# Optimization experiments

Hardware: AMD Instinct MI355X
Metric: run time of the kernel (lower is better)

The kernel has to match this reference:

```python
import jax, jax.numpy as jnp
import numpy as np

B, N, H, P, R = 16, 256, 768, 2048, 3


def setup_inputs() -> dict:
    key = jax.random.key(0)
    ks = jax.random.split(key, 7)
    s_h = 1.0 / np.sqrt(H)
    s_p = 1.0 / np.sqrt(P)
    return {
        "features": jax.random.normal(ks[0], (B, N, H), dtype=jnp.float32),
        "head_W": jax.random.uniform(ks[1], (P, H), jnp.float32, -s_h, s_h),
        "head_b": jax.random.uniform(ks[2], (P,), jnp.float32, -s_h, s_h),
        "tail_W": jax.random.uniform(ks[3], (P, H), jnp.float32, -s_h, s_h),
        "tail_b": jax.random.uniform(ks[4], (P,), jnp.float32, -s_h, s_h),
        "bil_W": jax.random.uniform(ks[5], (R, P, P), jnp.float32, -s_p, s_p),
        "bil_b": jax.random.uniform(ks[6], (R,), jnp.float32, -s_p, s_p),
    }


def reference(features, head_W, head_b, tail_W, tail_b, bil_W, bil_b):
    # Linear projections (dropout is identity in eval mode)
    head = jnp.einsum("bnh,ph->bnp", features, head_W) + head_b  # [B,N,P]
    tail = jnp.einsum("bnh,ph->bnp", features, tail_W) + tail_b  # [B,N,P]
    # Bilinear over all region pairs, without materializing [B,N,N,P]:
    # first contract head with W[r] -> [B,N,R,P], then with tail -> [B,N,N,R]
    hw = jnp.einsum("bnp,rpq->bnrq", head, bil_W)                # [B,N,R,P]
    logits = jnp.einsum("bnrq,bmq->bnmr", hw, tail) + bil_b      # [B,N,N,R]
    return logits
```

## Files before the change

### kernel.cpp

```cpp
#include <hip/hip_runtime.h>

constexpr int Bb = 16;
constexpr int Nn = 256;
constexpr int Hh = 768;
constexpr int Pp = 2048;
constexpr int Rr = 3;
constexpr int Mm = Bb * Nn;
constexpr int HA = 896;
constexpr int KA = 2080;
constexpr int JA = Rr * HA;

typedef __bf16 bf16_t;
typedef __bf16 bf16x8 __attribute__((ext_vector_type(8)));
typedef __bf16 bf16x4 __attribute__((ext_vector_type(4)));
typedef float  floatx4 __attribute__((ext_vector_type(4)));

__device__ __forceinline__ void gld_lds16(const void* g, void* l) {
    __builtin_amdgcn_global_load_lds(
        (__attribute__((address_space(1))) void*)g,
        (__attribute__((address_space(3))) void*)l,
        16, 0, 0);
}

__global__ __launch_bounds__(256) void build_Faug(
    const float* __restrict__ F, bf16_t* __restrict__ out)
{
    const int idx = blockIdx.x * 256 + threadIdx.x;
    const int n = idx / (HA / 4), c4 = idx % (HA / 4);
    const int h = c4 * 4;
    bf16x4 o;
    if (h < Hh) {
        float4 v = *(const float4*)(F + (size_t)n * Hh + h);
        o = { (bf16_t)v.x, (bf16_t)v.y, (bf16_t)v.z, (bf16_t)v.w };
    } else {
        #pragma unroll
        for (int e = 0; e < 4; ++e) o[e] = (bf16_t)((h + e == Hh) ? 1.0f : 0.0f);
    }
    *(bf16x4*)(out + (size_t)n * HA + h) = o;
}

__global__ __launch_bounds__(256) void build_tWaug(
    const float* __restrict__ tW, const float* __restrict__ bt,
    bf16_t* __restrict__ out)
{
    __shared__ float t[32][33];
    const int j0 = blockIdx.y * 32, q0 = blockIdx.x * 32;
    const int tx = threadIdx.x, ty = threadIdx.y;
    #pragma unroll
    for (int s = 0; s < 4; ++s) {
        const int q = q0 + ty + s * 8, j = j0 + tx;
        t[ty + s * 8][tx] = (j < Hh) ? tW[(size_t)q * Hh + j] : 0.0f;
    }
    __syncthreads();
    #pragma unroll
    for (int s = 0; s < 4; ++s) {
        const int j = j0 + ty + s * 8, q = q0 + tx;
        float v = t[tx][ty + s * 8];
        if (j == Hh) v = bt[q];
        else if (j > Hh) v = 0.0f;
        out[(size_t)j * Pp + q] = (bf16_t)v;
    }
}

__global__ __launch_bounds__(256) void build_hWaug(
    const float* __restrict__ hW, const float* __restrict__ bh,
    bf16_t* __restrict__ out)
{
    __shared__ float t[32][33];
    const int h0 = blockIdx.y * 32, p0 = blockIdx.x * 32;
    const int tx = threadIdx.x, ty = threadIdx.y;
    #pragma unroll
    for (int s = 0; s < 4; ++s) {
        const int p = p0 + ty + s * 8, h = h0 + tx;
        t[ty + s * 8][tx] = (p < Pp && h < Hh) ? hW[(size_t)p * Hh + h] : 0.0f;
    }
    __syncthreads();
    #pragma unroll
    for (int s = 0; s < 4; ++s) {
        const int h = h0 + ty + s * 8, p = p0 + tx;
        float v = t[tx][ty + s * 8];
        if (h == Hh) v = (p < Pp) ? bh[p] : (p == Pp ? 1.0f : 0.0f);
        else if (h > Hh) v = 0.0f;
        out[(size_t)h * KA + p] = (bf16_t)v;
    }
}

__global__ __launch_bounds__(256) void fill_T1cols(
    const float* __restrict__ bil_b, bf16_t* __restrict__ T1)
{
    const int idx = blockIdx.x * 256 + threadIdx.x;
    if (idx >= Rr * HA) return;
    const int r = idx / HA, j = idx % HA;
    bf16_t* p = T1 + (size_t)r * HA * KA + (size_t)j * KA + Pp;
    p[0] = (bf16_t)(j == Hh ? bil_b[r] : 0.0f);
    #pragma unroll
    for (int e = 1; e < 32; ++e) p[e] = (bf16_t)0.0f;
}

__global__ __launch_bounds__(256) void gemm_nt_128x64_bf32(
    const bf16_t* __restrict__ A, int lda,
    const float*  __restrict__ B, int ldb, size_t sB,
    bf16_t* __restrict__ C, int ldc, size_t sC, int K)
{
    B += (size_t)blockIdx.z * sB;
    C += (size_t)blockIdx.z * sC;

    __shared__ bf16_t As[2][128 * 32];
    __shared__ float  Bs[2][64 * 32];

    const int tid = threadIdx.x;
    const int w = tid >> 6;
    const int l = tid & 63;
    const int m0 = blockIdx.y * 128;
    const int n0 = blockIdx.x * 64;

    const bf16_t* ga0 = A + (size_t)(m0 + (w << 4) + (l >> 2)) * lda + ((l & 3) << 3);
    const bf16_t* ga1 = ga0 + (size_t)64 * lda;
    const int brow = (w << 3) + (l >> 3);
    const int bgrp = (l & 7) ^ (l >> 3);
    const float* gb0 = B + (size_t)(n0 + brow) * ldb + (bgrp << 2);
    const float* gb1 = gb0 + (size_t)32 * ldb;

    const int wm = (w >> 1) << 6;
    const int wn = (w & 1) << 5;
    const int fr = l & 15;
    const int fq = (l >> 4) << 3;

    const int swz = fr & 7;
    const int cg0 = (l >> 4) << 1;
    const int off0 = ((cg0 ^ swz) << 2);
    const int off1 = (((cg0 + 1) ^ swz) << 2);

    floatx4 acc[4][2] = {};

    {
        gld_lds16(ga0, (char*)As[0] + (w << 10));
        gld_lds16(ga1, (char*)As[0] + 4096 + (w << 10));
        gld_lds16(gb0, (char*)Bs[0] + (w << 10));
        gld_lds16(gb1, (char*)Bs[0] + 4096 + (w << 10));
        ga0 += 32; ga1 += 32; gb0 += 32; gb1 += 32;
    }

    const int steps = K >> 5;
    for (int k = 0; k < steps; ++k) {
        __syncthreads();
        const int cur = k & 1;
        if (k + 1 < steps) {
            gld_lds16(ga0, (char*)As[cur ^ 1] + (w << 10));
            gld_lds16(ga1, (char*)As[cur ^ 1] + 4096 + (w << 10));
            gld_lds16(gb0, (char*)Bs[cur ^ 1] + (w << 10));
            gld_lds16(gb1, (char*)Bs[cur ^ 1] + 4096 + (w << 10));
            ga0 += 32; ga1 += 32; gb0 += 32; gb1 += 32;
        }

        bf16x8 a[4], b[2];
        #pragma unroll
        for (int i = 0; i < 4; ++i)
            a[i] = *(const bf16x8*)&As[cur][(wm + i * 16 + fr) * 32 + fq];
        #pragma unroll
        for (int j = 0; j < 2; ++j) {
            const float* bp = &Bs[cur][(wn + j * 16 + fr) * 32];
            floatx4 x0 = *(const floatx4*)(bp + off0);
            floatx4 x1 = *(const floatx4*)(bp + off1);
            #pragma unroll
            for (int e = 0; e < 4; ++e) { b[j][e] = (bf16_t)x0[e]; b[j][e + 4] = (bf16_t)x1[e]; }
        }
        #pragma unroll
        for (int i = 0; i < 4; ++i)
            #pragma unroll
            for (int j = 0; j < 2; ++j)
                acc[i][j] = __builtin_amdgcn_mfma_f32_16x16x32_bf16(a[i], b[j], acc[i][j], 0, 0, 0);
    }

    const int em = m0 + wm + ((l >> 4) << 2);
    const int en = n0 + wn + (l & 15);
    #pragma unroll
    for (int i = 0; i < 4; ++i)
        #pragma unroll
        for (int j = 0; j < 2; ++j)
            #pragma unroll
            for (int rg = 0; rg < 4; ++rg)
                C[(size_t)(em + i * 16 + rg) * ldc + en + j * 16] = (bf16_t)acc[i][j][rg];
}

__global__ __launch_bounds__(256) void gemm_nt_64(
    const bf16_t* __restrict__ A, int lda, size_t sA,
    const bf16_t* __restrict__ B, int ldb, size_t sB,
    bf16_t* __restrict__ C, int ldc, size_t sC, int K)
{
    A += (size_t)blockIdx.z * sA;
    B += (size_t)blockIdx.z * sB;
    C += (size_t)blockIdx.z * sC;

    __shared__ bf16_t As[2][64 * 32];
    __shared__ bf16_t Bs[2][64 * 32];

    const int tid = threadIdx.x;
    const int w = tid >> 6;
    const int l = tid & 63;
    const int m0 = blockIdx.y * 64;
    const int n0 = blockIdx.x * 64;

    const bf16_t* ga = A + (size_t)(m0 + (tid >> 2)) * lda + ((tid & 3) << 3);
    const bf16_t* gb = B + (size_t)(n0 + (tid >> 2)) * ldb + ((tid & 3) << 3);

    const int wm = (w >> 1) << 5;
    const int wn = (w & 1) << 5;
    const int fr = l & 15;
    const int fq = (l >> 4) << 3;

    floatx4 acc[2][2] = {};

    {
        gld_lds16(ga, (char*)As[0] + (w << 10));
        gld_lds16(gb, (char*)Bs[0] + (w << 10));
        ga += 32; gb += 32;
    }

    const int steps = K >> 5;
    for (int k = 0; k < steps; ++k) {
        __syncthreads();
        const int cur = k & 1;
        if (k + 1 < steps) {
            gld_lds16(ga, (char*)As[cur ^ 1] + (w << 10));
            gld_lds16(gb, (char*)Bs[cur ^ 1] + (w << 10));
            ga += 32; gb += 32;
        }

        bf16x8 a[2], b[2];
        #pragma unroll
        for (int i = 0; i < 2; ++i) {
            a[i] = *(const bf16x8*)&As[cur][(wm + i * 16 + fr) * 32 + fq];
            b[i] = *(const bf16x8*)&Bs[cur][(wn + i * 16 + fr) * 32 + fq];
        }
        #pragma unroll
        for (int i = 0; i < 2; ++i)
            #pragma unroll
            for (int j = 0; j < 2; ++j)
                acc[i][j] = __builtin_amdgcn_mfma_f32_16x16x32_bf16(a[i], b[j], acc[i][j], 0, 0, 0);
    }

    const int em = m0 + wm + ((l >> 4) << 2);
    const int en = n0 + wn + (l & 15);
    #pragma unroll
    for (int i = 0; i < 2; ++i)
        #pragma unroll
        for (int j = 0; j < 2; ++j)
            #pragma unroll
            for (int rg = 0; rg < 4; ++rg)
                C[(size_t)(em + i * 16 + rg) * ldc + en + j * 16] = (bf16_t)acc[i][j][rg];
}

__global__ __launch_bounds__(256) void gemm_nt_128(
    const bf16_t* __restrict__ A, int lda,
    const bf16_t* __restrict__ B, int ldb,
    bf16_t* __restrict__ C, int ldc, int K)
{
    __shared__ bf16_t As[2][128 * 32];
    __shared__ bf16_t Bs[2][128 * 32];

    const int tid = threadIdx.x;
    const int w = tid >> 6;
    const int l = tid & 63;
    const int m0 = blockIdx.y * 128;
    const int n0 = blockIdx.x * 128;

    const int srow = (w << 4) + (l >> 2);
    const int scol = (l & 3) << 3;
    const bf16_t* ga0 = A + (size_t)(m0 + srow) * lda + scol;
    const bf16_t* ga1 = ga0 + (size_t)64 * lda;
    const bf16_t* gb0 = B + (size_t)(n0 + srow) * ldb + scol;
    const bf16_t* gb1 = gb0 + (size_t)64 * ldb;

    const int wm = (w >> 1) << 6;
    const int wn = (w & 1) << 6;
    const int fr = l & 15;
    const int fq = (l >> 4) << 3;

    floatx4 acc[4][4] = {};

    {
        char* a = (char*)As[0] + (w << 10);
        char* b = (char*)Bs[0] + (w << 10);
        gld_lds16(ga0, a); gld_lds16(ga1, a + 4096);
        gld_lds16(gb0, b); gld_lds16(gb1, b + 4096);
        ga0 += 32; ga1 += 32; gb0 += 32; gb1 += 32;
    }

    const int steps = K >> 5;
    for (int k = 0; k < steps; ++k) {
        __syncthreads();
        const int cur = k & 1;
        if (k + 1 < steps) {
            char* a = (char*)As[cur ^ 1] + (w << 10);
            char* b = (char*)Bs[cur ^ 1] + (w << 10);
            gld_lds16(ga0, a); gld_lds16(ga1, a + 4096);
            gld_lds16(gb0, b); gld_lds16(gb1, b + 4096);
            ga0 += 32; ga1 += 32; gb0 += 32; gb1 += 32;
        }

        bf16x8 a[4], b[4];
        #pragma unroll
        for (int i = 0; i < 4; ++i) {
            a[i] = *(const bf16x8*)&As[cur][(wm + i * 16 + fr) * 32 + fq];
            b[i] = *(const bf16x8*)&Bs[cur][(wn + i * 16 + fr) * 32 + fq];
        }
        #pragma unroll
        for (int i = 0; i < 4; ++i)
            #pragma unroll
            for (int j = 0; j < 4; ++j)
                acc[i][j] = __builtin_amdgcn_mfma_f32_16x16x32_bf16(a[i], b[j], acc[i][j], 0, 0, 0);
    }

    const int em = m0 + wm + ((l >> 4) << 2);
    const int en = n0 + wn + (l & 15);
    #pragma unroll
    for (int j = 0; j < 4; ++j) {
        const int n = en + j * 16;
        #pragma unroll
        for (int i = 0; i < 4; ++i) {
            #pragma unroll
            for (int rg = 0; rg < 4; ++rg)
                C[(size_t)(em + i * 16 + rg) * ldc + n] = (bf16_t)(acc[i][j][rg]);
        }
    }
}

__global__ __launch_bounds__(512) void gemm_out_fused(
    const bf16_t* __restrict__ FG,
    const bf16_t* __restrict__ FA,
    float* __restrict__ OUT)
{
    __shared__ bf16_t S[2][4][64 * 32];

    const int b = blockIdx.z;
    const int n0 = blockIdx.y * 64;
    const int m0 = blockIdx.x * 64;

    const int tid = threadIdx.x;
    const int w = tid >> 6;
    const int l = tid & 63;

    const int srow = ((w & 3) << 4) + (l >> 2);
    const int scol = (l & 3) << 3;
    const int t0 = w >> 2;
    const bf16_t* g0 = FG + (size_t)(b * Nn + n0 + srow) * JA + t0 * HA + scol;
    const bf16_t* g1 = (t0 == 0)
        ? FG + (size_t)(b * Nn + n0 + srow) * JA + 2 * HA + scol
        : FA + (size_t)(b * Nn + m0 + srow) * HA + scol;

    const int n_off = (w >> 2) << 5;
    const int m_off = (w & 3) << 4;
    const int fr = l & 15;
    const int fq = (l >> 4) << 3;

    floatx4 acc[Rr][2] = {};

    {
        char* base = (char*)&S[0][0][0];
        gld_lds16(g0, base + (w << 10));        g0 += 32;
        gld_lds16(g1, base + 8192 + (w << 10)); g1 += 32;
    }

    constexpr int STEPS = HA / 32;
    for (int k = 0; k < STEPS; ++k) {
        __syncthreads();
        const int cur = k & 1;
        if (k + 1 < STEPS) {
            char* base = (char*)&S[cur ^ 1][0][0];
            gld_lds16(g0, base + (w << 10));        g0 += 32;
            gld_lds16(g1, base + 8192 + (w << 10)); g1 += 32;
        }

        bf16x8 t = *(const bf16x8*)&S[cur][3][(m_off + fr) * 32 + fq];
        #pragma unroll
        for (int r = 0; r < Rr; ++r) {
            #pragma unroll
            for (int i = 0; i < 2; ++i) {
                bf16x8 a = *(const bf16x8*)&S[cur][r][(n_off + i * 16 + fr) * 32 + fq];
                acc[r][i] = __builtin_amdgcn_mfma_f32_16x16x32_bf16(a, t, acc[r][i], 0, 0, 0);
            }
        }
    }

    const int en_ = n0 + n_off + ((l >> 4) << 2);
    const int em_ = m0 + m_off + (l & 15);
    #pragma unroll
    for (int i = 0; i < 2; ++i)
        #pragma unroll
        for (int rg = 0; rg < 4; ++rg) {
            const int n = en_ + i * 16 + rg;
            float* o = OUT + (((size_t)b * Nn + n) * Nn + em_) * Rr;
            #pragma unroll
            for (int r = 0; r < Rr; ++r)
                o[r] = acc[r][i][rg];
        }
}

extern "C" void kernel_launch(void* const* d_in, const int* in_sizes, int n_in,
                              void* d_out, int out_size, void* d_ws, size_t ws_size,
                              hipStream_t stream) {
    const float* features = (const float*)d_in[0];
    const float* head_W   = (const float*)d_in[1];
    const float* head_b   = (const float*)d_in[2];
    const float* tail_W   = (const float*)d_in[3];
    const float* tail_b   = (const float*)d_in[4];
    const float* bil_W    = (const float*)d_in[5];
    const float* bil_b    = (const float*)d_in[6];
    float* out = (float*)d_out;

    char* ws = (char*)d_ws;
    bf16_t* Faug   = (bf16_t*)ws;  ws += (size_t)Mm * HA * 2;
    bf16_t* tWaug  = (bf16_t*)ws;  ws += (size_t)HA * Pp * 2;
    bf16_t* hWaug  = (bf16_t*)ws;  ws += (size_t)HA * KA * 2;
    bf16_t* T1taug = (bf16_t*)ws;  ws += (size_t)Rr * HA * KA * 2;
    bf16_t* Bop    = (bf16_t*)ws;  ws += (size_t)Rr * HA * HA * 2;
    bf16_t* FG     = (bf16_t*)ws;  ws += (size_t)Mm * JA * 2;

    build_Faug<<<Mm * (HA / 4) / 256, 256, 0, stream>>>(features, Faug);
    build_tWaug<<<dim3(Pp / 32, HA / 32), dim3(32, 8), 0, stream>>>(tail_W, tail_b, tWaug);
    build_hWaug<<<dim3(KA / 32, HA / 32), dim3(32, 8), 0, stream>>>(head_W, head_b, hWaug);

    gemm_nt_128x64_bf32<<<dim3(Pp / 64, HA / 128, Rr), 256, 0, stream>>>(
        tWaug, Pp,
        bil_W, Pp, (size_t)Pp * Pp,
        T1taug, KA, (size_t)HA * KA, Pp);
    fill_T1cols<<<(Rr * HA + 255) / 256, 256, 0, stream>>>(bil_b, T1taug);

    gemm_nt_64<<<dim3(HA / 64, HA / 64, Rr), 256, 0, stream>>>(
        T1taug, KA, (size_t)HA * KA,
        hWaug, KA, 0,
        Bop, HA, (size_t)HA * HA, KA);

    gemm_nt_128<<<dim3(JA / 128, Mm / 128), 256, 0, stream>>>(
        Faug, HA,
        Bop, HA,
        FG, JA, HA);

    gemm_out_fused<<<dim3(Nn / 64, Nn / 64, Bb), 512, 0, stream>>>(FG, Faug, out);
}
```

Before: 262.5 us.

## Deepen GEMM LDS pipelines to four stages with explicit vmcnt waits

Each GEMM kernel moves from a double-buffered LDS pipeline to a four-buffer ring that prefetches three K-steps ahead. Every iteration now issues an explicit s_waitcnt vmcnt so that only the current stage's global-to-LDS loads must have landed, followed by a raw barrier. The aim is to hide more global memory latency behind the MFMA work. In exchange LDS use per block doubles, which can reduce occupancy, especially for the 128x128 kernel at 64KB.

```diff
diff --git a/kernel.cpp b/kernel.cpp
--- a/kernel.cpp
+++ b/kernel.cpp
@@ -22,6 +22,14 @@
         16, 0, 0);
 }
 
+#define WAIT_VMCNT(n) asm volatile("s_waitcnt vmcnt(" #n ")" ::: "memory")
+
+__device__ __forceinline__ void pipe_barrier() {
+    __builtin_amdgcn_s_barrier();
+    __builtin_amdgcn_sched_barrier(0);
+    asm volatile("" ::: "memory");
+}
+
 __global__ __launch_bounds__(256) void build_Faug(
     const float* __restrict__ F, bf16_t* __restrict__ out)
 {
@@ -105,8 +113,8 @@
     B += (size_t)blockIdx.z * sB;
     C += (size_t)blockIdx.z * sC;
 
-    __shared__ bf16_t As[2][128 * 32];
-    __shared__ float  Bs[2][64 * 32];
+    __shared__ bf16_t As[4][128 * 32];
+    __shared__ float  Bs[4][64 * 32];
 
     const int tid = threadIdx.x;
     const int w = tid >> 6;
@@ -133,23 +141,29 @@
 
     floatx4 acc[4][2] = {};
 
-    {
-        gld_lds16(ga0, (char*)As[0] + (w << 10));
-        gld_lds16(ga1, (char*)As[0] + 4096 + (w << 10));
-        gld_lds16(gb0, (char*)Bs[0] + (w << 10));
-        gld_lds16(gb1, (char*)Bs[0] + 4096 + (w << 10));
+    #pragma unroll
+    for (int t = 0; t < 3; ++t) {
+        gld_lds16(ga0, (char*)As[t] + (w << 10));
+        gld_lds16(ga1, (char*)As[t] + 4096 + (w << 10));
+        gld_lds16(gb0, (char*)Bs[t] + (w << 10));
+        gld_lds16(gb1, (char*)Bs[t] + 4096 + (w << 10));
         ga0 += 32; ga1 += 32; gb0 += 32; gb1 += 32;
     }
 
     const int steps = K >> 5;
     for (int k = 0; k < steps; ++k) {
-        __syncthreads();
-        const int cur = k & 1;
-        if (k + 1 < steps) {
-            gld_lds16(ga0, (char*)As[cur ^ 1] + (w << 10));
-            gld_lds16(ga1, (char*)As[cur ^ 1] + 4096 + (w << 10));
-            gld_lds16(gb0, (char*)Bs[cur ^ 1] + (w << 10));
-            gld_lds16(gb1, (char*)Bs[cur ^ 1] + 4096 + (w << 10));
+        if (k + 2 < steps)      WAIT_VMCNT(8);
+        else if (k + 1 < steps) WAIT_VMCNT(4);
+        else                    WAIT_VMCNT(0);
+        pipe_barrier();
+
+        const int cur = k & 3;
+        if (k + 3 < steps) {
+            const int nxt = (k + 3) & 3;
+            gld_lds16(ga0, (char*)As[nxt] + (w << 10));
+            gld_lds16(ga1, (char*)As[nxt] + 4096 + (w << 10));
+            gld_lds16(gb0, (char*)Bs[nxt] + (w << 10));
+            gld_lds16(gb1, (char*)Bs[nxt] + 4096 + (w << 10));
             ga0 += 32; ga1 += 32; gb0 += 32; gb1 += 32;
         }
 
@@ -192,8 +206,8 @@
     B += (size_t)blockIdx.z * sB;
     C += (size_t)blockIdx.z * sC;
 
-    __shared__ bf16_t As[2][64 * 32];
-    __shared__ bf16_t Bs[2][64 * 32];
+    __shared__ bf16_t As[4][64 * 32];
+    __shared__ bf16_t Bs[4][64 * 32];
 
     const int tid = threadIdx.x;
     const int w = tid >> 6;
@@ -211,19 +225,25 @@
 
     floatx4 acc[2][2] = {};
 
-    {
-        gld_lds16(ga, (char*)As[0] + (w << 10));
-        gld_lds16(gb, (char*)Bs[0] + (w << 10));
+    #pragma unroll
+    for (int t = 0; t < 3; ++t) {
+        gld_lds16(ga, (char*)As[t] + (w << 10));
+        gld_lds16(gb, (char*)Bs[t] + (w << 10));
         ga += 32; gb += 32;
     }
 
     const int steps = K >> 5;
     for (int k = 0; k < steps; ++k) {
-        __syncthreads();
-        const int cur = k & 1;
-        if (k + 1 < steps) {
-            gld_lds16(ga, (char*)As[cur ^ 1] + (w << 10));
-            gld_lds16(gb, (char*)Bs[cur ^ 1] + (w << 10));
+        if (k + 2 < steps)      WAIT_VMCNT(4);
+        else if (k + 1 < steps) WAIT_VMCNT(2);
+        else                    WAIT_VMCNT(0);
+        pipe_barrier();
+
+        const int cur = k & 3;
+        if (k + 3 < steps) {
+            const int nxt = (k + 3) & 3;
+            gld_lds16(ga, (char*)As[nxt] + (w << 10));
+            gld_lds16(gb, (char*)Bs[nxt] + (w << 10));
             ga += 32; gb += 32;
         }
 
@@ -256,8 +276,8 @@
     const bf16_t* __restrict__ B, int ldb,
     bf16_t* __restrict__ C, int ldc, int K)
 {
-    __shared__ bf16_t As[2][128 * 32];
-    __shared__ bf16_t Bs[2][128 * 32];
+    __shared__ bf16_t As[4][128 * 32];
+    __shared__ bf16_t Bs[4][128 * 32];
 
     const int tid = threadIdx.x;
     const int w = tid >> 6;
@@ -279,9 +299,10 @@
 
     floatx4 acc[4][4] = {};
 
-    {
-        char* a = (char*)As[0] + (w << 10);
-        char* b = (char*)Bs[0] + (w << 10);
+    #pragma unroll
+    for (int t = 0; t < 3; ++t) {
+        char* a = (char*)As[t] + (w << 10);
+        char* b = (char*)Bs[t] + (w << 10);
         gld_lds16(ga0, a); gld_lds16(ga1, a + 4096);
         gld_lds16(gb0, b); gld_lds16(gb1, b + 4096);
         ga0 += 32; ga1 += 32; gb0 += 32; gb1 += 32;
@@ -289,11 +310,16 @@
 
     const int steps = K >> 5;
     for (int k = 0; k < steps; ++k) {
-        __syncthreads();
-        const int cur = k & 1;
-        if (k + 1 < steps) {
-            char* a = (char*)As[cur ^ 1] + (w << 10);
-            char* b = (char*)Bs[cur ^ 1] + (w << 10);
+        if (k + 2 < steps)      WAIT_VMCNT(8);
+        else if (k + 1 < steps) WAIT_VMCNT(4);
+        else                    WAIT_VMCNT(0);
+        pipe_barrier();
+
+        const int cur = k & 3;
+        if (k + 3 < steps) {
+            const int nxt = (k + 3) & 3;
+            char* a = (char*)As[nxt] + (w << 10);
+            char* b = (char*)Bs[nxt] + (w << 10);
             gld_lds16(ga0, a); gld_lds16(ga1, a + 4096);
             gld_lds16(gb0, b); gld_lds16(gb1, b + 4096);
             ga0 += 32; ga1 += 32; gb0 += 32; gb1 += 32;
@@ -331,7 +357,7 @@
     const bf16_t* __restrict__ FA,
     float* __restrict__ OUT)
 {
-    __shared__ bf16_t S[2][4][64 * 32];
+    __shared__ bf16_t S[4][4][64 * 32];
 
     const int b = blockIdx.z;
     const int n0 = blockIdx.y * 64;
@@ -356,18 +382,23 @@
 
     floatx4 acc[Rr][2] = {};
 
-    {
-        char* base = (char*)&S[0][0][0];
+    #pragma unroll
+    for (int t = 0; t < 3; ++t) {
+        char* base = (char*)&S[t][0][0];
         gld_lds16(g0, base + (w << 10));        g0 += 32;
         gld_lds16(g1, base + 8192 + (w << 10)); g1 += 32;
     }
 
     constexpr int STEPS = HA / 32;
     for (int k = 0; k < STEPS; ++k) {
-        __syncthreads();
-        const int cur = k & 1;
-        if (k + 1 < STEPS) {
-            char* base = (char*)&S[cur ^ 1][0][0];
+        if (k + 2 < STEPS)      WAIT_VMCNT(4);
+        else if (k + 1 < STEPS) WAIT_VMCNT(2);
+        else                    WAIT_VMCNT(0);
+        pipe_barrier();
+
+        const int cur = k & 3;
+        if (k + 3 < STEPS) {
+            char* base = (char*)&S[(k + 3) & 3][0][0];
             gld_lds16(g0, base + (w << 10));        g0 += 32;
             gld_lds16(g1, base + 8192 + (w << 10)); g1 += 32;
         }
```

Measured after the change: 313.6 us. 19.5% more time.

## Double K tile to 64 with XOR-swizzled LDS across all GEMM kernels

Applied to the files above, without the earlier changes.

Every GEMM kernel now stages 64-wide K slices instead of 32, halving the number of barriers and loop iterations, and uses an XOR swizzle on LDS column groups to avoid bank conflicts on the wider rows. The padded K dimension grows to a multiple of 64 and the bias/zero column fill is widened to match. The T1 and FG workspace buffers are aliased to reduce footprint. The cost is doubled LDS usage per block, which may lower occupancy.

```diff
diff --git a/kernel.cpp b/kernel.cpp
--- a/kernel.cpp
+++ b/kernel.cpp
@@ -7,7 +7,7 @@
 constexpr int Rr = 3;
 constexpr int Mm = Bb * Nn;
 constexpr int HA = 896;
-constexpr int KA = 2080;
+constexpr int KA = 2112;
 constexpr int JA = Rr * HA;
 
 typedef __bf16 bf16_t;
@@ -21,6 +21,7 @@
         (__attribute__((address_space(3))) void*)l,
         16, 0, 0);
 }
+
 
 __global__ __launch_bounds__(256) void build_Faug(
     const float* __restrict__ F, bf16_t* __restrict__ out)
@@ -94,7 +95,7 @@
     bf16_t* p = T1 + (size_t)r * HA * KA + (size_t)j * KA + Pp;
     p[0] = (bf16_t)(j == Hh ? bil_b[r] : 0.0f);
     #pragma unroll
-    for (int e = 1; e < 32; ++e) p[e] = (bf16_t)0.0f;
+    for (int e = 1; e < 64; ++e) p[e] = (bf16_t)0.0f;
 }
 
 __global__ __launch_bounds__(256) void gemm_nt_128x64_bf32(
@@ -105,8 +106,8 @@
     B += (size_t)blockIdx.z * sB;
     C += (size_t)blockIdx.z * sC;
 
-    __shared__ bf16_t As[2][128 * 32];
-    __shared__ float  Bs[2][64 * 32];
+    __shared__ bf16_t As[2][128 * 64];
+    __shared__ float  Bs[2][64 * 64];
 
     const int tid = threadIdx.x;
     const int w = tid >> 6;
@@ -114,66 +115,70 @@
     const int m0 = blockIdx.y * 128;
     const int n0 = blockIdx.x * 64;
 
-    const bf16_t* ga0 = A + (size_t)(m0 + (w << 4) + (l >> 2)) * lda + ((l & 3) << 3);
-    const bf16_t* ga1 = ga0 + (size_t)64 * lda;
-    const int brow = (w << 3) + (l >> 3);
-    const int bgrp = (l & 7) ^ (l >> 3);
-    const float* gb0 = B + (size_t)(n0 + brow) * ldb + (bgrp << 2);
-    const float* gb1 = gb0 + (size_t)32 * ldb;
+    const bf16_t* ga = A + (size_t)(m0 + (w << 3) + (l >> 3)) * lda
+                         + (((l & 7) ^ (l >> 3)) << 3);
+    {
+    }
+    const int br7 = ((w & 1) << 2) | (l >> 4);
+    const int p15 = l & 15;
+    const float* gb = B + (size_t)(n0 + (w << 2) + (l >> 4)) * ldb
+                        + ((p15 >> 3) << 5) + (((p15 & 7) ^ br7) << 2);
 
     const int wm = (w >> 1) << 6;
     const int wn = (w & 1) << 5;
     const int fr = l & 15;
-    const int fq = (l >> 4) << 3;
-
-    const int swz = fr & 7;
-    const int cg0 = (l >> 4) << 1;
-    const int off0 = ((cg0 ^ swz) << 2);
-    const int off1 = (((cg0 + 1) ^ swz) << 2);
+    const int hi = l >> 4;
+    const int f7 = fr & 7;
 
     floatx4 acc[4][2] = {};
 
     {
-        gld_lds16(ga0, (char*)As[0] + (w << 10));
-        gld_lds16(ga1, (char*)As[0] + 4096 + (w << 10));
-        gld_lds16(gb0, (char*)Bs[0] + (w << 10));
-        gld_lds16(gb1, (char*)Bs[0] + 4096 + (w << 10));
-        ga0 += 32; ga1 += 32; gb0 += 32; gb1 += 32;
-    }
-
-    const int steps = K >> 5;
+        #pragma unroll
+        for (int i = 0; i < 4; ++i) {
+            gld_lds16(ga + (size_t)(i * 32) * lda, (char*)As[0] + i * 4096 + (w << 10));
+            gld_lds16(gb + (size_t)(i * 16) * ldb, (char*)Bs[0] + i * 4096 + (w << 10));
+        }
+        ga += 64; gb += 64;
+    }
+
+    const int steps = K >> 6;
     for (int k = 0; k < steps; ++k) {
         __syncthreads();
         const int cur = k & 1;
         if (k + 1 < steps) {
-            gld_lds16(ga0, (char*)As[cur ^ 1] + (w << 10));
-            gld_lds16(ga1, (char*)As[cur ^ 1] + 4096 + (w << 10));
-            gld_lds16(gb0, (char*)Bs[cur ^ 1] + (w << 10));
-            gld_lds16(gb1, (char*)Bs[cur ^ 1] + 4096 + (w << 10));
-            ga0 += 32; ga1 += 32; gb0 += 32; gb1 += 32;
-        }
-
-        bf16x8 a[4], b[2];
-        #pragma unroll
-        for (int i = 0; i < 4; ++i)
-            a[i] = *(const bf16x8*)&As[cur][(wm + i * 16 + fr) * 32 + fq];
-        #pragma unroll
-        for (int j = 0; j < 2; ++j) {
-            const float* bp = &Bs[cur][(wn + j * 16 + fr) * 32];
-            floatx4 x0 = *(const floatx4*)(bp + off0);
-            floatx4 x1 = *(const floatx4*)(bp + off1);
-            #pragma unroll
-            for (int e = 0; e < 4; ++e) { b[j][e] = (bf16_t)x0[e]; b[j][e + 4] = (bf16_t)x1[e]; }
-        }
-        #pragma unroll
-        for (int i = 0; i < 4; ++i)
-            #pragma unroll
-            for (int j = 0; j < 2; ++j)
-                acc[i][j] = __builtin_amdgcn_mfma_f32_16x16x32_bf16(a[i], b[j], acc[i][j], 0, 0, 0);
-    }
-
-    const int em = m0 + wm + ((l >> 4) << 2);
-    const int en = n0 + wn + (l & 15);
+            #pragma unroll
+            for (int i = 0; i < 4; ++i) {
+                gld_lds16(ga + (size_t)(i * 32) * lda, (char*)As[cur ^ 1] + i * 4096 + (w << 10));
+                gld_lds16(gb + (size_t)(i * 16) * ldb, (char*)Bs[cur ^ 1] + i * 4096 + (w << 10));
+            }
+            ga += 64; gb += 64;
+        }
+
+        #pragma unroll
+        for (int kk = 0; kk < 2; ++kk) {
+            const int aph = ((((kk << 2) + hi) ^ f7) << 3);
+            bf16x8 a[4], b[2];
+            #pragma unroll
+            for (int i = 0; i < 4; ++i)
+                a[i] = *(const bf16x8*)&As[cur][(wm + i * 16 + fr) * 64 + aph];
+            #pragma unroll
+            for (int j = 0; j < 2; ++j) {
+                const float* bp = &Bs[cur][(wn + j * 16 + fr) * 64 + (kk << 5)];
+                floatx4 x0 = *(const floatx4*)(bp + (((hi << 1) ^ f7) << 2));
+                floatx4 x1 = *(const floatx4*)(bp + ((((hi << 1) + 1) ^ f7) << 2));
+                #pragma unroll
+                for (int e = 0; e < 4; ++e) { b[j][e] = (bf16_t)x0[e]; b[j][e + 4] = (bf16_t)x1[e]; }
+            }
+            #pragma unroll
+            for (int i = 0; i < 4; ++i)
+                #pragma unroll
+                for (int j = 0; j < 2; ++j)
+                    acc[i][j] = __builtin_amdgcn_mfma_f32_16x16x32_bf16(a[i], b[j], acc[i][j], 0, 0, 0);
+        }
+    }
+
+    const int em = m0 + wm + (hi << 2);
+    const int en = n0 + wn + fr;
     #pragma unroll
     for (int i = 0; i < 4; ++i)
         #pragma unroll
@@ -192,8 +197,8 @@
     B += (size_t)blockIdx.z * sB;
     C += (size_t)blockIdx.z * sC;
 
-    __shared__ bf16_t As[2][64 * 32];
-    __shared__ bf16_t Bs[2][64 * 32];
+    __shared__ bf16_t As[2][64 * 64];
+    __shared__ bf16_t Bs[2][64 * 64];
 
     const int tid = threadIdx.x;
     const int w = tid >> 6;
@@ -201,47 +206,60 @@
     const int m0 = blockIdx.y * 64;
     const int n0 = blockIdx.x * 64;
 
-    const bf16_t* ga = A + (size_t)(m0 + (tid >> 2)) * lda + ((tid & 3) << 3);
-    const bf16_t* gb = B + (size_t)(n0 + (tid >> 2)) * ldb + ((tid & 3) << 3);
+    const int srow = (w << 3) + (l >> 3);
+    const int scol = ((l & 7) ^ (l >> 3)) << 3;
+    const bf16_t* ga = A + (size_t)(m0 + srow) * lda + scol;
+    const bf16_t* gb = B + (size_t)(n0 + srow) * ldb + scol;
 
     const int wm = (w >> 1) << 5;
     const int wn = (w & 1) << 5;
     const int fr = l & 15;
-    const int fq = (l >> 4) << 3;
+    const int hi = l >> 4;
+    const int f7 = fr & 7;
 
     floatx4 acc[2][2] = {};
 
     {
-        gld_lds16(ga, (char*)As[0] + (w << 10));
-        gld_lds16(gb, (char*)Bs[0] + (w << 10));
-        ga += 32; gb += 32;
-    }
-
-    const int steps = K >> 5;
+        #pragma unroll
+        for (int i = 0; i < 2; ++i) {
+            gld_lds16(ga + (size_t)(i * 32) * lda, (char*)As[0] + i * 4096 + (w << 10));
+            gld_lds16(gb + (size_t)(i * 32) * ldb, (char*)Bs[0] + i * 4096 + (w << 10));
+        }
+        ga += 64; gb += 64;
+    }
+
+    const int steps = K >> 6;
     for (int k = 0; k < steps; ++k) {
         __syncthreads();
         const int cur = k & 1;
         if (k + 1 < steps) {
-            gld_lds16(ga, (char*)As[cur ^ 1] + (w << 10));
-            gld_lds16(gb, (char*)Bs[cur ^ 1] + (w << 10));
-            ga += 32; gb += 32;
-        }
-
-        bf16x8 a[2], b[2];
-        #pragma unroll
-        for (int i = 0; i < 2; ++i) {
-            a[i] = *(const bf16x8*)&As[cur][(wm + i * 16 + fr) * 32 + fq];
-            b[i] = *(const bf16x8*)&Bs[cur][(wn + i * 16 + fr) * 32 + fq];
-        }
-        #pragma unroll
-        for (int i = 0; i < 2; ++i)
-            #pragma unroll
-            for (int j = 0; j < 2; ++j)
-                acc[i][j] = __builtin_amdgcn_mfma_f32_16x16x32_bf16(a[i], b[j], acc[i][j], 0, 0, 0);
-    }
-
-    const int em = m0 + wm + ((l >> 4) << 2);
-    const int en = n0 + wn + (l & 15);
+            #pragma unroll
+            for (int i = 0; i < 2; ++i) {
+                gld_lds16(ga + (size_t)(i * 32) * lda, (char*)As[cur ^ 1] + i * 4096 + (w << 10));
+                gld_lds16(gb + (size_t)(i * 32) * ldb, (char*)Bs[cur ^ 1] + i * 4096 + (w << 10));
+            }
+            ga += 64; gb += 64;
+        }
+
+        #pragma unroll
+        for (int kk = 0; kk < 2; ++kk) {
+            const int ph = ((((kk << 2) + hi) ^ f7) << 3);
+            bf16x8 a[2], b[2];
+            #pragma unroll
+            for (int i = 0; i < 2; ++i) {
+                a[i] = *(const bf16x8*)&As[cur][(wm + i * 16 + fr) * 64 + ph];
+                b[i] = *(const bf16x8*)&Bs[cur][(wn + i * 16 + fr) * 64 + ph];
+            }
+            #pragma unroll
+            for (int i = 0; i < 2; ++i)
+                #pragma unroll
+                for (int j = 0; j < 2; ++j)
+                    acc[i][j] = __builtin_amdgcn_mfma_f32_16x16x32_bf16(a[i], b[j], acc[i][j], 0, 0, 0);
+        }
+    }
+
+    const int em = m0 + wm + (hi << 2);
+    const int en = n0 + wn + fr;
     #pragma unroll
     for (int i = 0; i < 2; ++i)
         #pragma unroll
@@ -256,8 +274,8 @@
     const bf16_t* __restrict__ B, int ldb,
     bf16_t* __restrict__ C, int ldc, int K)
 {
-    __shared__ bf16_t As[2][128 * 32];
-    __shared__ bf16_t Bs[2][128 * 32];
+    __shared__ bf16_t As[2][128 * 64];
+    __shared__ bf16_t Bs[2][128 * 64];
 
     const int tid = threadIdx.x;
     const int w = tid >> 6;
@@ -265,55 +283,60 @@
     const int m0 = blockIdx.y * 128;
     const int n0 = blockIdx.x * 128;
 
-    const int srow = (w << 4) + (l >> 2);
-    const int scol = (l & 3) << 3;
-    const bf16_t* ga0 = A + (size_t)(m0 + srow) * lda + scol;
-    const bf16_t* ga1 = ga0 + (size_t)64 * lda;
-    const bf16_t* gb0 = B + (size_t)(n0 + srow) * ldb + scol;
-    const bf16_t* gb1 = gb0 + (size_t)64 * ldb;
+    const int srow = (w << 3) + (l >> 3);
+    const int scol = ((l & 7) ^ (l >> 3)) << 3;
+    const bf16_t* ga = A + (size_t)(m0 + srow) * lda + scol;
+    const bf16_t* gb = B + (size_t)(n0 + srow) * ldb + scol;
 
     const int wm = (w >> 1) << 6;
     const int wn = (w & 1) << 6;
     const int fr = l & 15;
-    const int fq = (l >> 4) << 3;
+    const int hi = l >> 4;
+    const int f7 = fr & 7;
 
     floatx4 acc[4][4] = {};
 
     {
-        char* a = (char*)As[0] + (w << 10);
-        char* b = (char*)Bs[0] + (w << 10);
-        gld_lds16(ga0, a); gld_lds16(ga1, a + 4096);
-        gld_lds16(gb0, b); gld_lds16(gb1, b + 4096);
-        ga0 += 32; ga1 += 32; gb0 += 32; gb1 += 32;
-    }
-
-    const int steps = K >> 5;
+        #pragma unroll
+        for (int i = 0; i < 4; ++i) {
+            gld_lds16(ga + (size_t)(i * 32) * lda, (char*)As[0] + i * 4096 + (w << 10));
+            gld_lds16(gb + (size_t)(i * 32) * ldb, (char*)Bs[0] + i * 4096 + (w << 10));
+        }
+        ga += 64; gb += 64;
+    }
+
+    const int steps = K >> 6;
     for (int k = 0; k < steps; ++k) {
         __syncthreads();
         const int cur = k & 1;
         if (k + 1 < steps) {
-            char* a = (char*)As[cur ^ 1] + (w << 10);
-            char* b = (char*)Bs[cur ^ 1] + (w << 10);
-            gld_lds16(ga0, a); gld_lds16(ga1, a + 4096);
-            gld_lds16(gb0, b); gld_lds16(gb1, b + 4096);
-            ga0 += 32; ga1 += 32; gb0 += 32; gb1 += 32;
-        }
-
-        bf16x8 a[4], b[4];
-        #pragma unroll
-        for (int i = 0; i < 4; ++i) {
-            a[i] = *(const bf16x8*)&As[cur][(wm + i * 16 + fr) * 32 + fq];
-            b[i] = *(const bf16x8*)&Bs[cur][(wn + i * 16 + fr) * 32 + fq];
-        }
-        #pragma unroll
-        for (int i = 0; i < 4; ++i)
-            #pragma unroll
-            for (int j = 0; j < 4; ++j)
-                acc[i][j] = __builtin_amdgcn_mfma_f32_16x16x32_bf16(a[i], b[j], acc[i][j], 0, 0, 0);
-    }
-
-    const int em = m0 + wm + ((l >> 4) << 2);
-    const int en = n0 + wn + (l & 15);
+            #pragma unroll
+            for (int i = 0; i < 4; ++i) {
+                gld_lds16(ga + (size_t)(i * 32) * lda, (char*)As[cur ^ 1] + i * 4096 + (w << 10));
+                gld_lds16(gb + (size_t)(i * 32) * ldb, (char*)Bs[cur ^ 1] + i * 4096 + (w << 10));
+            }
+            ga += 64; gb += 64;
+        }
+
+        #pragma unroll
+        for (int kk = 0; kk < 2; ++kk) {
+            const int ph = ((((kk << 2) + hi) ^ f7) << 3);
+            bf16x8 a[4], b[4];
+            #pragma unroll
+            for (int i = 0; i < 4; ++i) {
+                a[i] = *(const bf16x8*)&As[cur][(wm + i * 16 + fr) * 64 + ph];
+                b[i] = *(const bf16x8*)&Bs[cur][(wn + i * 16 + fr) * 64 + ph];
+            }
+            #pragma unroll
+            for (int i = 0; i < 4; ++i)
+                #pragma unroll
+                for (int j = 0; j < 4; ++j)
+                    acc[i][j] = __builtin_amdgcn_mfma_f32_16x16x32_bf16(a[i], b[j], acc[i][j], 0, 0, 0);
+        }
+    }
+
+    const int em = m0 + wm + (hi << 2);
+    const int en = n0 + wn + fr;
     #pragma unroll
     for (int j = 0; j < 4; ++j) {
         const int n = en + j * 16;
@@ -331,7 +354,7 @@
     const bf16_t* __restrict__ FA,
     float* __restrict__ OUT)
 {
-    __shared__ bf16_t S[2][4][64 * 32];
+    __shared__ bf16_t S[2][4][64 * 64];
 
     const int b = blockIdx.z;
     const int n0 = blockIdx.y * 64;
@@ -341,50 +364,60 @@
     const int w = tid >> 6;
     const int l = tid & 63;
 
-    const int srow = ((w & 3) << 4) + (l >> 2);
-    const int scol = (l & 3) << 3;
-    const int t0 = w >> 2;
-    const bf16_t* g0 = FG + (size_t)(b * Nn + n0 + srow) * JA + t0 * HA + scol;
-    const bf16_t* g1 = (t0 == 0)
-        ? FG + (size_t)(b * Nn + n0 + srow) * JA + 2 * HA + scol
-        : FA + (size_t)(b * Nn + m0 + srow) * HA + scol;
+    const int srow = (w << 3) + (l >> 3);
+    const int scol = ((l & 7) ^ (l >> 3)) << 3;
+    const bf16_t* g0 = FG + (size_t)(b * Nn + n0 + srow) * JA + 0 * HA + scol;
+    const bf16_t* g1 = FG + (size_t)(b * Nn + n0 + srow) * JA + 1 * HA + scol;
+    const bf16_t* g2 = FG + (size_t)(b * Nn + n0 + srow) * JA + 2 * HA + scol;
+    const bf16_t* g3 = FA + (size_t)(b * Nn + m0 + srow) * HA + scol;
 
     const int n_off = (w >> 2) << 5;
     const int m_off = (w & 3) << 4;
     const int fr = l & 15;
-    const int fq = (l >> 4) << 3;
+    const int hi = l >> 4;
+    const int f7 = fr & 7;
 
     floatx4 acc[Rr][2] = {};
 
     {
         char* base = (char*)&S[0][0][0];
-        gld_lds16(g0, base + (w << 10));        g0 += 32;
-        gld_lds16(g1, base + 8192 + (w << 10)); g1 += 32;
-    }
-
-    constexpr int STEPS = HA / 32;
+        gld_lds16(g0, base + 0 * 8192 + (w << 10));
+        gld_lds16(g1, base + 1 * 8192 + (w << 10));
+        gld_lds16(g2, base + 2 * 8192 + (w << 10));
+        gld_lds16(g3, base + 3 * 8192 + (w << 10));
+        g0 += 64; g1 += 64; g2 += 64; g3 += 64;
+    }
+
+    constexpr int STEPS = HA / 64;
     for (int k = 0; k < STEPS; ++k) {
         __syncthreads();
         const int cur = k & 1;
         if (k + 1 < STEPS) {
             char* base = (char*)&S[cur ^ 1][0][0];
-            gld_lds16(g0, base + (w << 10));        g0 += 32;
-            gld_lds16(g1, base + 8192 + (w << 10)); g1 += 32;
-        }
-
-        bf16x8 t = *(const bf16x8*)&S[cur][3][(m_off + fr) * 32 + fq];
-        #pragma unroll
-        for (int r = 0; r < Rr; ++r) {
-            #pragma unroll
-            for (int i = 0; i < 2; ++i) {
-                bf16x8 a = *(const bf16x8*)&S[cur][r][(n_off + i * 16 + fr) * 32 + fq];
-                acc[r][i] = __builtin_amdgcn_mfma_f32_16x16x32_bf16(a, t, acc[r][i], 0, 0, 0);
-            }
-        }
-    }
-
-    const int en_ = n0 + n_off + ((l >> 4) << 2);
-    const int em_ = m0 + m_off + (l & 15);
+            gld_lds16(g0, base + 0 * 8192 + (w << 10));
+            gld_lds16(g1, base + 1 * 8192 + (w << 10));
+            gld_lds16(g2, base + 2 * 8192 + (w << 10));
+            gld_lds16(g3, base + 3 * 8192 + (w << 10));
+            g0 += 64; g1 += 64; g2 += 64; g3 += 64;
+        }
+
+        #pragma unroll
+        for (int kk = 0; kk < 2; ++kk) {
+            const int ph = ((((kk << 2) + hi) ^ f7) << 3);
+            bf16x8 t = *(const bf16x8*)&S[cur][3][(m_off + fr) * 64 + ph];
+            #pragma unroll
+            for (int r = 0; r < Rr; ++r) {
+                #pragma unroll
+                for (int i = 0; i < 2; ++i) {
+                    bf16x8 a = *(const bf16x8*)&S[cur][r][(n_off + i * 16 + fr) * 64 + ph];
+                    acc[r][i] = __builtin_amdgcn_mfma_f32_16x16x32_bf16(a, t, acc[r][i], 0, 0, 0);
+                }
+            }
+        }
+    }
+
+    const int en_ = n0 + n_off + (hi << 2);
+    const int em_ = m0 + m_off + fr;
     #pragma unroll
     for (int i = 0; i < 2; ++i)
         #pragma unroll
@@ -413,9 +446,9 @@
     bf16_t* Faug   = (bf16_t*)ws;  ws += (size_t)Mm * HA * 2;
     bf16_t* tWaug  = (bf16_t*)ws;  ws += (size_t)HA * Pp * 2;
     bf16_t* hWaug  = (bf16_t*)ws;  ws += (size_t)HA * KA * 2;
-    bf16_t* T1taug = (bf16_t*)ws;  ws += (size_t)Rr * HA * KA * 2;
     bf16_t* Bop    = (bf16_t*)ws;  ws += (size_t)Rr * HA * HA * 2;
-    bf16_t* FG     = (bf16_t*)ws;  ws += (size_t)Mm * JA * 2;
+    bf16_t* T1taug = (bf16_t*)ws;
+    bf16_t* FG     = T1taug;
 
     build_Faug<<<Mm * (HA / 4) / 256, 256, 0, stream>>>(features, Faug);
     build_tWaug<<<dim3(Pp / 32, HA / 32), dim3(32, 8), 0, stream>>>(tail_W, tail_b, tWaug);
```

Result: no change. 265.3 us (+1.1%).
